# Performance work log

Hardware: AMD Instinct MI355X
Metric: run time of the kernel (lower is better)

## Reference

```python
import jax, jax.numpy as jnp
import numpy as np

EPS = 1e-5
MODES = 64
KERNEL = 25
PRED = 336
N_ENC = 2

def rmsnorm(x, w):
    return x * jax.lax.rsqrt(jnp.mean(jnp.square(x), axis=-1, keepdims=True) + EPS) * w

def ffn(x, w1, b1, w2, b2):
    return jax.nn.gelu(x @ w1 + b1, approximate=False) @ w2 + b2

def series_decomp(x):
    # moving average with zero padding (Conv1d, kernel=KERNEL, weight=1/KERNEL)
    pad = (KERNEL - 1) // 2
    xp = jnp.pad(x, ((0, 0), (pad, pad), (0, 0)))
    cs = jnp.cumsum(xp, axis=1)
    cs = jnp.concatenate([jnp.zeros_like(cs[:, :1]), cs], axis=1)
    t = (cs[:, KERNEL:, :] - cs[:, :-KERNEL, :]) / KERNEL  # [B,T,C]
    return x - t, t

def fourier_block(x, w, nw):
    # x: [B,T,C]; w: [MODES,C,2] learned complex weights; nw: [C] rms scale
    B, T, C = x.shape
    Xf = jnp.fft.rfft(x, axis=1)                      # [B,F,C] complex64
    mag = jnp.sum(Xf[:, 1:].real**2 + Xf[:, 1:].imag**2, axis=-1)  # [B,F-1]
    K = min(MODES, Xf.shape[1] - 1)
    _, idx = jax.lax.top_k(mag, K)
    idx = idx + 1                                      # skip DC, [B,K]
    Xsel = jnp.take_along_axis(Xf, idx[:, :, None], axis=1)  # [B,K,C]
    Wc = w[:K, :, 0] + 1j * w[:K, :, 1]               # [K,C]
    Ysel = Xsel * Wc[None]                             # [B,K,C]
    Yf = jnp.zeros_like(Xf).at[jnp.arange(B)[:, None], idx].set(Ysel)
    y = jnp.fft.irfft(Yf, n=T, axis=1)                 # [B,T,C]
    return rmsnorm(y, nw)

def setup_inputs() -> dict:
    key = jax.random.key(0)
    ks = iter(jax.random.split(key, 64))
    B, L, Cin, Cout, D, FF = 32, 1024, 8, 8, 512, 2048
    r = lambda *s: jax.random.normal(next(ks), s, dtype=jnp.float32) * 0.02
    z = lambda *s: jnp.zeros(s, dtype=jnp.float32)
    o = lambda *s: jnp.ones(s, dtype=jnp.float32)
    return {
        'x': jax.random.normal(next(ks), (B, L, Cin), dtype=jnp.float32),
        'enc_in_w': r(Cin, D), 'enc_in_b': z(D),
        'dec_in_w': r(Cin, D), 'dec_in_b': z(D),
        'enc_freq_w': r(N_ENC, MODES, D, 2), 'enc_freq_nw': o(N_ENC, D),
        'enc_n1': o(N_ENC, D), 'enc_n2': o(N_ENC, D),
        'enc_w1': r(N_ENC, D, FF), 'enc_b1': z(N_ENC, FF),
        'enc_w2': r(N_ENC, FF, D), 'enc_b2': z(N_ENC, D),
        'dec_freq_w': r(MODES, D, 2), 'dec_freq_nw': o(D),
        'dec_n1': o(D), 'dec_n2': o(D), 'dec_nx': o(D),
        'dec_cross_w': r(D, D), 'dec_cross_b': z(D),
        'dec_w1': r(D, FF), 'dec_b1': z(FF),
        'dec_w2': r(FF, D), 'dec_b2': z(D),
        'seas_w': r(D, Cout), 'seas_b': z(Cout),
        'tr_w1': r(D, FF), 'tr_b1': z(FF),
        'tr_w2': r(FF, Cout), 'tr_b2': z(Cout),
        'mix_w': r(Cout, Cout), 'mix_b': z(Cout),
        'qpos': jax.random.normal(next(ks), (1, PRED, D), dtype=jnp.float32) * 0.02,
    }

def reference(x, enc_in_w, enc_in_b, dec_in_w, dec_in_b,
              enc_freq_w, enc_freq_nw, enc_n1, enc_n2, enc_w1, enc_b1, enc_w2, enc_b2,
              dec_freq_w, dec_freq_nw, dec_n1, dec_n2, dec_nx, dec_cross_w, dec_cross_b,
              dec_w1, dec_b1, dec_w2, dec_b2, seas_w, seas_b,
              tr_w1, tr_b1, tr_w2, tr_b2, mix_w, mix_b, qpos):
    s, t = series_decomp(x)
    sez = s @ enc_in_w + enc_in_b                      # [B,L,D]
    for i in range(N_ENC):
        sez = sez + fourier_block(rmsnorm(sez, enc_n1[i]), enc_freq_w[i], enc_freq_nw[i])
        sez = sez + ffn(rmsnorm(sez, enc_n2[i]), enc_w1[i], enc_b1[i], enc_w2[i], enc_b2[i])
    memory = sez
    tgt = qpos + sez[:, -1:, :]                        # [B,PRED,D]
    # decoder layer
    m = jnp.mean(memory, axis=1, keepdims=True)        # [B,1,D]
    m = rmsnorm(m, dec_nx) @ dec_cross_w + dec_cross_b
    y = fourier_block(rmsnorm(tgt, dec_n1), dec_freq_w, dec_freq_nw)
    xd = tgt + y * jax.nn.sigmoid(m)
    xd = xd + ffn(rmsnorm(xd, dec_n2), dec_w1, dec_b1, dec_w2, dec_b2)
    sez_out = xd @ seas_w + seas_b                     # [B,PRED,Cout]
    tr = t @ dec_in_w + dec_in_b
    tr_out = ffn(tr[:, -1:, :], tr_w1, tr_b1, tr_w2, tr_b2)  # [B,1,Cout], broadcasts
    out = sez_out + tr_out
    return out @ mix_w + mix_b
```

## Files before the change

### kernel.cpp

```cpp
#include <hip/hip_runtime.h>
#include <hip/hip_fp16.h>
#include <math.h>

#define B_    32
#define L_    1024
#define D_    512
#define FF_   2048
#define PRED_ 336
#define ME_   (B_*L_)
#define MD_   (B_*PRED_)
#define EPS_  1e-5f

typedef _Float16 f16;
typedef _Float16 f16x8 __attribute__((ext_vector_type(8)));
typedef float    f32x4 __attribute__((ext_vector_type(4)));

__device__ __forceinline__ float wred64(float v) {
#pragma unroll
  for (int o = 32; o > 0; o >>= 1) v += __shfl_xor(v, o, 64);
  return v;
}
__device__ __forceinline__ double dwred64(double v) {
#pragma unroll
  for (int o = 32; o > 0; o >>= 1) v += __shfl_xor(v, o, 64);
  return v;
}
__device__ __forceinline__ float gelu_f(float x) {
  return 0.5f * x * (1.0f + erff(x * 0.7071067811865476f));
}
__device__ __forceinline__ void gl2lds16(const void* g, void* l) {
  __builtin_amdgcn_global_load_lds((const __attribute__((address_space(1))) void*)g,
                                   (__attribute__((address_space(3))) void*)l, 16, 0, 0);
}

__global__ void k_transpose_cast(const float* __restrict__ in, f16* __restrict__ out, int R, int C) {
  __shared__ float t[32][33];
  int c0 = blockIdx.x * 32, r0 = blockIdx.y * 32;
  int tx = threadIdx.x, ty = threadIdx.y;
#pragma unroll
  for (int j = ty; j < 32; j += 8) t[j][tx] = in[(size_t)(r0 + j) * C + c0 + tx];
  __syncthreads();
#pragma unroll
  for (int j = ty; j < 32; j += 8) out[(size_t)(c0 + j) * R + r0 + tx] = (f16)t[tx][j];
}

__global__ __launch_bounds__(256) void k_decomp_proj(const float* __restrict__ x,
    const float* __restrict__ w, const float* __restrict__ bias, float* __restrict__ sez) {
  int b = blockIdx.x, t0 = blockIdx.y * 128, tid = threadIdx.x;
  __shared__ float xs[152][8];
  __shared__ float st[128][8];
  __shared__ float wsm[8 * 512];
  __shared__ float bs[512];
  for (int i = tid; i < 152 * 8; i += 256) {
    int tt = i >> 3, c = i & 7; int tg = t0 - 12 + tt;
    xs[tt][c] = (tg >= 0 && tg < 1024) ? x[((size_t)b * 1024 + tg) * 8 + c] : 0.0f;
  }
  for (int i = tid; i < 4096; i += 256) wsm[i] = w[i];
  for (int i = tid; i < 512; i += 256) bs[i] = bias[i];
  __syncthreads();
  for (int i = tid; i < 1024; i += 256) {
    int t = i >> 3, c = i & 7;
    float s = 0.f;
#pragma unroll
    for (int j = 0; j < 25; ++j) s += xs[t + j][c];
    st[t][c] = xs[t + 12][c] - s / 25.0f;
  }
  __syncthreads();
#pragma unroll
  for (int g = 0; g < 2; ++g) {
    int d = tid + g * 256;
    float wb[8];
#pragma unroll
    for (int c = 0; c < 8; ++c) wb[c] = wsm[c * 512 + d];
    float bb = bs[d];
    for (int t = 0; t < 128; ++t) {
      float o = bb;
#pragma unroll
      for (int c = 0; c < 8; ++c) o += st[t][c] * wb[c];
      sez[((size_t)b * 1024 + t0 + t) * 512 + d] = o;
    }
  }
}

__global__ __launch_bounds__(512) void k_trend_trin(const float* __restrict__ x, const float* __restrict__ w,
    const float* __restrict__ bias, float* __restrict__ trin) {
  int b = blockIdx.x, tid = threadIdx.x;
  __shared__ float tl[8];
  if (tid < 8) {
    float s = 0.f;
    for (int j = 1011; j <= 1023; ++j) s += x[((size_t)b * 1024 + j) * 8 + tid];
    tl[tid] = s / 25.0f;
  }
  __syncthreads();
  float acc = bias[tid];
#pragma unroll
  for (int c = 0; c < 8; ++c) acc += tl[c] * w[c * 512 + tid];
  trin[b * 512 + tid] = acc;
}

__global__ __launch_bounds__(256) void k_rinv(const float* __restrict__ xin, float* __restrict__ rinv) {
  int row = blockIdx.x * 4 + (threadIdx.x >> 6), lane = threadIdx.x & 63;
  const float4* p = (const float4*)(xin + (size_t)row * 512);
  float4 a = p[lane * 2], b = p[lane * 2 + 1];
  float ss = a.x*a.x + a.y*a.y + a.z*a.z + a.w*a.w + b.x*b.x + b.y*b.y + b.z*b.z + b.w*b.w;
  ss = wred64(ss);
  if (lane == 0) rinv[row] = rsqrtf(ss * (1.0f / 512.0f) + EPS_);
}

__global__ __launch_bounds__(256) void k_rms_f16(const float* __restrict__ xin, const float* __restrict__ w,
    f16* __restrict__ out) {
  int row = blockIdx.x * 4 + (threadIdx.x >> 6), lane = threadIdx.x & 63;
  const float4* p = (const float4*)(xin + (size_t)row * 512);
  float4 a = p[lane * 2], b = p[lane * 2 + 1];
  float ss = a.x*a.x + a.y*a.y + a.z*a.z + a.w*a.w + b.x*b.x + b.y*b.y + b.z*b.z + b.w*b.w;
  ss = wred64(ss);
  float ri = rsqrtf(ss * (1.0f / 512.0f) + EPS_);
  const float4* wp = (const float4*)w;
  float4 wa = wp[lane * 2], wb = wp[lane * 2 + 1];
  float va[8] = {a.x, a.y, a.z, a.w, b.x, b.y, b.z, b.w};
  float wv[8] = {wa.x, wa.y, wa.z, wa.w, wb.x, wb.y, wb.z, wb.w};
  f16x8 o;
#pragma unroll
  for (int j = 0; j < 8; ++j) o[j] = (f16)((va[j] * ri) * wv[j]);
  *(f16x8*)(out + (size_t)row * 512 + lane * 8) = o;
}

#define IDX_(i) ((i) + ((i) >> 4))
__global__ __launch_bounds__(256) void k_fft_enc(const float* __restrict__ sez, const float* __restrict__ rinv,
    const float* __restrict__ n1, float* __restrict__ Xf) {
  int b = blockIdx.x, c0 = blockIdx.y * 4, tid = threadIdx.x;
  __shared__ double Zr[2][1088], Zi[2][1088];
  __shared__ double TWr[256], TWi[256];
  if (tid < 256) {
    double a = -6.283185307179586232 * (double)tid / 1024.0;
    TWr[tid] = cos(a); TWi[tid] = sin(a);
  }
  for (int i = tid; i < 4096; i += 256) {
    int t = i >> 2, cl = i & 3;
    float xv = (sez[((size_t)b * 1024 + t) * 512 + c0 + cl] * rinv[b * 1024 + t]) * n1[c0 + cl];
    int u = t, rt = 0;
#pragma unroll
    for (int d = 0; d < 5; ++d) { rt = (rt << 2) | (u & 3); u >>= 2; }
    if (cl & 1) Zi[cl >> 1][IDX_(rt)] = (double)xv; else Zr[cl >> 1][IDX_(rt)] = (double)xv;
  }
  __syncthreads();
#pragma unroll
  for (int s = 0; s < 5; ++s) {
    const int lh = 2 * s, h = 1 << lh;
#pragma unroll
    for (int qi = 0; qi < 2; ++qi) {
      int q = tid + qi * 256;
      int p = q >> 8, qq = q & 255;
      int j = qq & (h - 1), g = qq >> lh;
      int p0 = (g << (lh + 2)) + j;
      int i0 = IDX_(p0), i1 = IDX_(p0 + h), i2 = IDX_(p0 + 2 * h), i3 = IDX_(p0 + 3 * h);
      int tw = j << (8 - lh);
      double w1r = TWr[tw], w1i = TWi[tw];
      double w2r = w1r * w1r - w1i * w1i, w2i = 2.0 * w1r * w1i;
      double w3r = w2r * w1r - w2i * w1i, w3i = w2r * w1i + w2i * w1r;
      double Ar = Zr[p][i0], Ai = Zi[p][i0];
      double br = Zr[p][i1], bi = Zi[p][i1];
      double cr = Zr[p][i2], ci = Zi[p][i2];
      double dr = Zr[p][i3], di = Zi[p][i3];
      double Br = br * w1r - bi * w1i, Bi = br * w1i + bi * w1r;
      double Cr = cr * w2r - ci * w2i, Ci = cr * w2i + ci * w2r;
      double Dr = dr * w3r - di * w3i, Di = dr * w3i + di * w3r;
      double T0r = Ar + Cr, T0i = Ai + Ci;
      double T1r = Ar - Cr, T1i = Ai - Ci;
      double T2r = Br + Dr, T2i = Bi + Di;
      double T3r = Bi - Di, T3i = Dr - Br;
      Zr[p][i0] = T0r + T2r; Zi[p][i0] = T0i + T2i;
      Zr[p][i1] = T1r + T3r; Zi[p][i1] = T1i + T3i;
      Zr[p][i2] = T0r - T2r; Zi[p][i2] = T0i - T2i;
      Zr[p][i3] = T1r - T3r; Zi[p][i3] = T1i - T3i;
    }
    __syncthreads();
  }
  for (int i = tid; i < 513 * 2; i += 256) {
    int f = i >> 1, p = i & 1;
    int mf = (1024 - f) & 1023;
    double Ar = Zr[p][IDX_(f)], Ai = Zi[p][IDX_(f)], Br = Zr[p][IDX_(mf)], Bi = Zi[p][IDX_(mf)];
    float4 o;
    o.x = (float)(0.5 * (Ar + Br)); o.y = (float)(0.5 * (Ai - Bi));
    o.z = (float)(0.5 * (Ai + Bi)); o.w = (float)(0.5 * (Br - Ar));
    *(float4*)&Xf[(((size_t)b * 513 + f) * 512 + c0 + 2 * p) * 2] = o;
  }
}

__global__ __launch_bounds__(256) void k_mag(const float* __restrict__ Xf, double* __restrict__ mag, int F) {
  int b = blockIdx.x, f = blockIdx.y + 1, tid = threadIdx.x;
  const float2* row = (const float2*)(Xf + ((size_t)b * F + f) * 512 * 2);
  double s = 0;
  for (int c = tid; c < 512; c += 256) { float2 v = row[c]; s += (double)v.x * v.x + (double)v.y * v.y; }
  s = dwred64(s);
  __shared__ double ps[4];
  if ((tid & 63) == 0) ps[tid >> 6] = s;
  __syncthreads();
  if (tid == 0) mag[b * 513 + f] = ps[0] + ps[1] + ps[2] + ps[3];
}

__global__ __launch_bounds__(64) void k_topk(const double* __restrict__ mag, int* __restrict__ idx, int F) {
  int b = blockIdx.x, lane = threadIdx.x;
  double v[9];
#pragma unroll
  for (int j = 0; j < 9; ++j) {
    int s = j * 64 + lane;
    v[j] = (s >= 1 && s < F) ? mag[b * 513 + s] : -1e300;
  }
  for (int r = 0; r < 64; ++r) {
    double bv = -1e300; int bi = 0;
#pragma unroll
    for (int j = 0; j < 9; ++j)
      if (v[j] > bv) { bv = v[j]; bi = j * 64 + lane; }
#pragma unroll
    for (int o = 32; o > 0; o >>= 1) {
      double ov = __shfl_xor(bv, o, 64);
      int oi = __shfl_xor(bi, o, 64);
      if (ov > bv || (ov == bv && oi < bi)) { bv = ov; bi = oi; }
    }
    if (lane == 0) idx[b * 64 + r] = bi;
#pragma unroll
    for (int j = 0; j < 9; ++j)
      if (bi == j * 64 + lane) v[j] = -1e300;
  }
}

__global__ __launch_bounds__(512) void k_gather(const float* __restrict__ Xf, const int* __restrict__ idx,
    const float* __restrict__ fw, float* __restrict__ Ysel, int F, int T) {
  int b = blockIdx.x, k = blockIdx.y, c = threadIdx.x;
  int f = idx[b * 64 + k];
  float sc = (2 * f == T) ? (1.0f / (float)T) : (2.0f / (float)T);
  float2 xv = *(const float2*)&Xf[(((size_t)b * F + f) * 512 + c) * 2];
  float wr = fw[(k * 512 + c) * 2], wi = fw[(k * 512 + c) * 2 + 1];
  float yr = (xv.x * wr - xv.y * wi) * sc;
  float yi = (xv.x * wi + xv.y * wr) * sc;
  *(float2*)&Ysel[((size_t)(b * 64 + k) * 512 + c) * 2] = make_float2(yr, yi);
}

template <int T>
__global__ __launch_bounds__(256) void k_irfft(const float* __restrict__ Ysel, const int* __restrict__ idx,
    const float* __restrict__ nw, const float* __restrict__ sig,
    float* __restrict__ dst, int mode) {
  int b = blockIdx.x, t0 = blockIdx.y * 16, tid = threadIdx.x;
  int cq = tid & 127;
  int tg = tid >> 7;
  __shared__ float tcT[16][68], tsT[16][68];
  __shared__ int sidx[64];
  __shared__ float red[4][8];
  __shared__ float rfac[16];
  if (tid < 64) sidx[tid] = idx[b * 64 + tid];
  __syncthreads();
  for (int i = tid; i < 1024; i += 256) {
    int k = i >> 4, tt = i & 15;
    int m = (sidx[k] * (t0 + tt)) % T;
    float ang = (float)m * (float)(6.283185307179586232 / (double)T);
    tcT[tt][k] = cosf(ang);
    tsT[tt][k] = sinf(ang);
  }
  __syncthreads();
  float acc[8][4];
#pragma unroll
  for (int q = 0; q < 8; ++q)
#pragma unroll
    for (int j = 0; j < 4; ++j) acc[q][j] = 0.f;
  const float4* ys = (const float4*)Ysel + (size_t)b * 64 * 256 + 2 * cq;
  for (int k4 = 0; k4 < 64; k4 += 4) {
    float4 ya[4], yb[4];
#pragma unroll
    for (int kk = 0; kk < 4; ++kk) {
      ya[kk] = ys[(size_t)(k4 + kk) * 256];
      yb[kk] = ys[(size_t)(k4 + kk) * 256 + 1];
    }
#pragma unroll
    for (int q = 0; q < 8; ++q) {
      int tt = tg * 8 + q;
      float4 c4 = *(const float4*)&tcT[tt][k4];
      float4 s4 = *(const float4*)&tsT[tt][k4];
      acc[q][0] += ya[0].x * c4.x - ya[0].y * s4.x;
      acc[q][1] += ya[0].z * c4.x - ya[0].w * s4.x;
      acc[q][2] += yb[0].x * c4.x - yb[0].y * s4.x;
      acc[q][3] += yb[0].z * c4.x - yb[0].w * s4.x;
      acc[q][0] += ya[1].x * c4.y - ya[1].y * s4.y;
      acc[q][1] += ya[1].z * c4.y - ya[1].w * s4.y;
      acc[q][2] += yb[1].x * c4.y - yb[1].y * s4.y;
      acc[q][3] += yb[1].z * c4.y - yb[1].w * s4.y;
      acc[q][0] += ya[2].x * c4.z - ya[2].y * s4.z;
      acc[q][1] += ya[2].z * c4.z - ya[2].w * s4.z;
      acc[q][2] += yb[2].x * c4.z - yb[2].y * s4.z;
      acc[q][3] += yb[2].z * c4.z - yb[2].w * s4.z;
      acc[q][0] += ya[3].x * c4.w - ya[3].y * s4.w;
      acc[q][1] += ya[3].z * c4.w - ya[3].w * s4.w;
      acc[q][2] += yb[3].x * c4.w - yb[3].y * s4.w;
      acc[q][3] += yb[3].z * c4.w - yb[3].w * s4.w;
    }
  }
  int lane = tid & 63, wv = tid >> 6;
#pragma unroll
  for (int q = 0; q < 8; ++q) {
    float v = wred64(acc[q][0] * acc[q][0] + acc[q][1] * acc[q][1]
                   + acc[q][2] * acc[q][2] + acc[q][3] * acc[q][3]);
    if (lane == 0) red[wv][q] = v;
  }
  __syncthreads();
  if (tid < 16) {
    int tg2 = tid >> 3, q = tid & 7;
    float s = red[tg2 * 2][q] + red[tg2 * 2 + 1][q];
    rfac[tid] = rsqrtf(s * (1.0f / 512.0f) + EPS_);
  }
  __syncthreads();
  int c = 4 * cq;
  float4 wc = *(const float4*)&nw[c];
  float4 sg = (mode == 1) ? *(const float4*)&sig[b * 512 + c] : make_float4(1.f, 1.f, 1.f, 1.f);
  float* drow = dst + ((size_t)b * T + t0) * 512 + c;
#pragma unroll
  for (int q = 0; q < 8; ++q) {
    int tt = tg * 8 + q;
    float rf = rfac[tt];
    float4 cur = *(float4*)&drow[(size_t)tt * 512];
    float y0 = (acc[q][0] * rf) * wc.x;
    float y1 = (acc[q][1] * rf) * wc.y;
    float y2 = (acc[q][2] * rf) * wc.z;
    float y3 = (acc[q][3] * rf) * wc.w;
    cur.x += (mode == 1) ? y0 * sg.x : y0;
    cur.y += (mode == 1) ? y1 * sg.y : y1;
    cur.z += (mode == 1) ? y2 * sg.z : y2;
    cur.w += (mode == 1) ? y3 * sg.w : y3;
    *(float4*)&drow[(size_t)tt * 512] = cur;
  }
}

template <int MODE>
__global__ __launch_bounds__(256) void k_gemm(const f16* __restrict__ A, const f16* __restrict__ Bt,
    const float* __restrict__ bias, float* __restrict__ Cf, f16* __restrict__ Ch,
    int M, int N, int K) {
  __shared__ f16 lA[2][128][64];
  __shared__ f16 lB[2][128][64];
  int bm = blockIdx.x, bn = blockIdx.y;
  int tid = threadIdx.x, lane = tid & 63, w = tid >> 6;
  int wr = w >> 1, wcq = w & 1;
  f32x4 acc[4][4];
#pragma unroll
  for (int i = 0; i < 4; ++i)
#pragma unroll
    for (int j = 0; j < 4; ++j) acc[i][j] = (f32x4){0.f, 0.f, 0.f, 0.f};
  int lr = lane >> 3;
  int kk = (lane & 7) * 8;
  int nk = K >> 6;
  auto STAGE = [&](int buf, int kt) {
#pragma unroll
    for (int i = 0; i < 4; ++i) {
      int rt = (w * 4 + i) * 8;
      int rr = rt + lr;
      gl2lds16(A + (size_t)(bm * 128 + rr) * K + kt * 64 + kk, &lA[buf][rt][0]);
      gl2lds16(Bt + (size_t)(bn * 128 + rr) * K + kt * 64 + kk, &lB[buf][rt][0]);
    }
  };
  STAGE(0, 0);
  int cur = 0;
  for (int kt = 0; kt < nk; ++kt) {
    if (kt + 1 < nk) {
      STAGE(cur ^ 1, kt + 1);
      asm volatile("s_waitcnt vmcnt(8)\n\ts_barrier" ::: "memory");
    } else {
      asm volatile("s_waitcnt vmcnt(0)\n\ts_barrier" ::: "memory");
    }
#pragma unroll
    for (int ki = 0; ki < 2; ++ki) {
      f16x8 af[4], bf[4];
#pragma unroll
      for (int mi = 0; mi < 4; ++mi)
        af[mi] = *(const f16x8*)&lA[cur][wr * 64 + mi * 16 + (lane & 15)][ki * 32 + (lane >> 4) * 8];
#pragma unroll
      for (int ni = 0; ni < 4; ++ni)
        bf[ni] = *(const f16x8*)&lB[cur][wcq * 64 + ni * 16 + (lane & 15)][ki * 32 + (lane >> 4) * 8];
#pragma unroll
      for (int mi = 0; mi < 4; ++mi)
#pragma unroll
        for (int ni = 0; ni < 4; ++ni)
          acc[mi][ni] = __builtin_amdgcn_mfma_f32_16x16x32_f16(af[mi], bf[ni], acc[mi][ni], 0, 0, 0);
    }
    asm volatile("s_barrier" ::: "memory");
    cur ^= 1;
  }
  int cbase = bn * 128 + wcq * 64;
  int rbase = bm * 128 + wr * 64;
#pragma unroll
  for (int mi = 0; mi < 4; ++mi)
#pragma unroll
    for (int ni = 0; ni < 4; ++ni) {
      int cg = cbase + ni * 16 + (lane & 15);
      float bv = bias[cg];
#pragma unroll
      for (int q = 0; q < 4; ++q) {
        int rg = rbase + mi * 16 + (lane >> 4) * 4 + q;
        float val = acc[mi][ni][q] + bv;
        if (MODE == 0) Ch[(size_t)rg * N + cg] = (f16)gelu_f(val);
        else           Cf[(size_t)rg * N + cg] += val;
      }
    }
}

__global__ __launch_bounds__(256) void k_mc_part(const float* __restrict__ sez, float* __restrict__ mcp) {
  int b = blockIdx.x, ch = blockIdx.y, tid = threadIdx.x;
  for (int d = tid; d < 512; d += 256) {
    float s = 0.f;
    for (int t = 0; t < 128; ++t) s += sez[((size_t)b * 1024 + ch * 128 + t) * 512 + d];
    mcp[((size_t)b * 8 + ch) * 512 + d] = s;
  }
}
__global__ __launch_bounds__(512) void k_mc_fin(const float* __restrict__ mcp, const float* __restrict__ nx,
    const float* __restrict__ Wc, const float* __restrict__ cb, float* __restrict__ sig) {
  int b = blockIdx.x, d = threadIdx.x;
  float m = 0.f;
#pragma unroll
  for (int ch = 0; ch < 8; ++ch) m += mcp[((size_t)b * 8 + ch) * 512 + d];
  m *= (1.0f / 1024.0f);
  float ss = wred64(m * m);
  __shared__ float ps[8];
  __shared__ float mn[512];
  int lane = d & 63, wv = d >> 6;
  if (lane == 0) ps[wv] = ss;
  __syncthreads();
  float tot = 0.f;
#pragma unroll
  for (int i = 0; i < 8; ++i) tot += ps[i];
  float ri = rsqrtf(tot * (1.0f / 512.0f) + EPS_);
  mn[d] = (m * ri) * nx[d];
  __syncthreads();
  float accv = cb[d];
  for (int e = 0; e < 512; ++e) accv += mn[e] * Wc[(size_t)e * 512 + d];
  sig[b * 512 + d] = 1.0f / (1.0f + expf(-accv));
}

__global__ __launch_bounds__(512) void k_make_tgt(const float* __restrict__ sez, const float* __restrict__ qpos,
    const float* __restrict__ n1, float* __restrict__ tgt, float* __restrict__ tgt_n,
    float* __restrict__ rinvd) {
  int row = blockIdx.x, d = threadIdx.x;
  int b = row / 336, p = row % 336;
  float v = qpos[(size_t)p * 512 + d] + sez[((size_t)b * 1024 + 1023) * 512 + d];
  tgt[(size_t)row * 512 + d] = v;
  float ss = wred64(v * v);
  __shared__ float ps[8];
  if ((d & 63) == 0) ps[d >> 6] = ss;
  __syncthreads();
  float t = 0.f;
#pragma unroll
  for (int i = 0; i < 8; ++i) t += ps[i];
  float ri = rsqrtf(t * (1.0f / 512.0f) + EPS_);
  tgt_n[(size_t)row * 512 + d] = (v * ri) * n1[d];
  if (d == 0) rinvd[row] = ri;
}

__global__ void k_dtab(float* __restrict__ dtt) {
  int f = blockIdx.x;
  for (int t = threadIdx.x; t < 336; t += 256) {
    float cv = 0.f, sv = 0.f;
    if (f < 169) {
      int m = (f * t) % 336;
      double a = 6.283185307179586232 * (double)m / 336.0;
      cv = (float)cos(a); sv = (float)sin(a);
    }
    dtt[((size_t)t * 176 + f) * 2]     = cv;
    dtt[((size_t)t * 176 + f) * 2 + 1] = sv;
  }
}
__global__ __launch_bounds__(512) void k_dft_dec(const float* __restrict__ tgt_n,
    const float* __restrict__ dtt, float* __restrict__ Xf) {
  int b = blockIdx.x, f0 = blockIdx.y * 4, c = threadIdx.x;
  float ar[4], ai[4];
#pragma unroll
  for (int i = 0; i < 4; ++i) { ar[i] = 0.f; ai[i] = 0.f; }
  const float* trow = tgt_n + (size_t)b * 336 * 512 + c;
  for (int t = 0; t < 336; ++t) {
    float xv = trow[(size_t)t * 512];
    const float* tab = dtt + ((size_t)t * 176 + f0) * 2;
#pragma unroll
    for (int ff = 0; ff < 4; ++ff) {
      ar[ff] += xv * tab[ff * 2];
      ai[ff] -= xv * tab[ff * 2 + 1];
    }
  }
#pragma unroll
  for (int ff = 0; ff < 4; ++ff) {
    int f = f0 + ff;
    if (f < 169)
      *(float2*)&Xf[(((size_t)b * 169 + f) * 512 + c) * 2] = make_float2(ar[ff], ai[ff]);
  }
}

__global__ __launch_bounds__(256) void k_tr_h(const float* __restrict__ trin, const float* __restrict__ w1,
    const float* __restrict__ b1, float* __restrict__ H) {
  int b = blockIdx.x, j0 = blockIdx.y * 512, tid = threadIdx.x;
  __shared__ float xs[512];
  for (int i = tid; i < 512; i += 256) xs[i] = trin[b * 512 + i];
  __syncthreads();
  int j = j0 + tid;
  float h0 = b1[j], h1 = b1[j + 256];
  const float* wp = w1 + j;
#pragma unroll 4
  for (int e = 0; e < 512; ++e) {
    float xe = xs[e];
    h0 += xe * wp[(size_t)e * 2048];
    h1 += xe * wp[(size_t)e * 2048 + 256];
  }
  H[b * 2048 + j] = gelu_f(h0);
  H[b * 2048 + j + 256] = gelu_f(h1);
}

__global__ __launch_bounds__(256) void k_tr_red(const float* __restrict__ H, const float* __restrict__ w2,
    const float* __restrict__ b2, float* __restrict__ trout) {
  int b = blockIdx.x, tid = threadIdx.x;
  __shared__ float red[4][8];
  float part[8];
#pragma unroll
  for (int co = 0; co < 8; ++co) part[co] = 0.f;
#pragma unroll
  for (int jj = 0; jj < 8; ++jj) {
    int j = tid + jj * 256;
    float g = H[b * 2048 + j];
    float4 wa = *(const float4*)&w2[(size_t)j * 8];
    float4 wb = *(const float4*)&w2[(size_t)j * 8 + 4];
    part[0] += g * wa.x; part[1] += g * wa.y; part[2] += g * wa.z; part[3] += g * wa.w;
    part[4] += g * wb.x; part[5] += g * wb.y; part[6] += g * wb.z; part[7] += g * wb.w;
  }
  int lane = tid & 63, wv = tid >> 6;
#pragma unroll
  for (int co = 0; co < 8; ++co) {
    float v = wred64(part[co]);
    if (lane == 0) red[wv][co] = v;
  }
  __syncthreads();
  if (tid < 8) trout[b * 8 + tid] = red[0][tid] + red[1][tid] + red[2][tid] + red[3][tid] + b2[tid];
}

__global__ __launch_bounds__(256) void k_head(const float* __restrict__ xd, const float* __restrict__ sw,
    const float* __restrict__ sb, const float* __restrict__ trout, const float* __restrict__ mw,
    const float* __restrict__ mb, float* __restrict__ outp) {
  int row = blockIdx.x, tid = threadIdx.x;
  int b = row / 336;
  __shared__ float wsm[512 * 8];
  __shared__ float red[4][8];
  __shared__ float srow[8];
  for (int i = tid; i < 4096; i += 256) wsm[i] = sw[i];
  __syncthreads();
  float part[8];
#pragma unroll
  for (int co = 0; co < 8; ++co) part[co] = 0.f;
#pragma unroll
  for (int g = 0; g < 2; ++g) {
    int d = tid + g * 256;
    float xv = xd[(size_t)row * 512 + d];
#pragma unroll
    for (int co = 0; co < 8; ++co) part[co] += xv * wsm[d * 8 + co];
  }
  int lane = tid & 63, wv = tid >> 6;
#pragma unroll
  for (int co = 0; co < 8; ++co) {
    float v = wred64(part[co]);
    if (lane == 0) red[wv][co] = v;
  }
  __syncthreads();
  if (tid == 0) {
#pragma unroll
    for (int co = 0; co < 8; ++co)
      srow[co] = red[0][co] + red[1][co] + red[2][co] + red[3][co] + sb[co] + trout[b * 8 + co];
  }
  __syncthreads();
  if (tid < 8) {
    float o = mb[tid];
#pragma unroll
    for (int co = 0; co < 8; ++co) o += srow[co] * mw[co * 8 + tid];
    outp[(size_t)row * 8 + tid] = o;
  }
}

extern "C" void kernel_launch(void* const* d_in, const int* in_sizes, int n_in,
                              void* d_out, int out_size, void* d_ws, size_t ws_size,
                              hipStream_t stream) {
  const float* x        = (const float*)d_in[0];
  const float* enc_in_w = (const float*)d_in[1];
  const float* enc_in_b = (const float*)d_in[2];
  const float* dec_in_w = (const float*)d_in[3];
  const float* dec_in_b = (const float*)d_in[4];
  const float* enc_fw   = (const float*)d_in[5];
  const float* enc_fnw  = (const float*)d_in[6];
  const float* enc_n1   = (const float*)d_in[7];
  const float* enc_n2   = (const float*)d_in[8];
  const float* enc_w1   = (const float*)d_in[9];
  const float* enc_b1   = (const float*)d_in[10];
  const float* enc_w2   = (const float*)d_in[11];
  const float* enc_b2   = (const float*)d_in[12];
  const float* dec_fw   = (const float*)d_in[13];
  const float* dec_fnw  = (const float*)d_in[14];
  const float* dec_n1   = (const float*)d_in[15];
  const float* dec_n2   = (const float*)d_in[16];
  const float* dec_nx   = (const float*)d_in[17];
  const float* dec_cw   = (const float*)d_in[18];
  const float* dec_cb   = (const float*)d_in[19];
  const float* dec_w1   = (const float*)d_in[20];
  const float* dec_b1   = (const float*)d_in[21];
  const float* dec_w2   = (const float*)d_in[22];
  const float* dec_b2   = (const float*)d_in[23];
  const float* seas_w   = (const float*)d_in[24];
  const float* seas_b   = (const float*)d_in[25];
  const float* tr_w1    = (const float*)d_in[26];
  const float* tr_b1    = (const float*)d_in[27];
  const float* tr_w2    = (const float*)d_in[28];
  const float* tr_b2    = (const float*)d_in[29];
  const float* mix_w    = (const float*)d_in[30];
  const float* mix_b    = (const float*)d_in[31];
  const float* qpos     = (const float*)d_in[32];
  float* outp = (float*)d_out;
  (void)in_sizes; (void)n_in; (void)out_size; (void)ws_size;

  char* wsb = (char*)d_ws;
  size_t off = 0;
  auto take = [&](size_t n) -> char* {
    char* p = wsb + off;
    off = (off + n + 255) & ~(size_t)255;
    return p;
  };
  float*  sez   = (float*)take((size_t)ME_ * 512 * 4);
  f16*    xn    = (f16*)take((size_t)ME_ * 512 * 2);
  const size_t XF_BYTES = (size_t)32 * 513 * 512 * 2 * 4;
  char*   arena = take(XF_BYTES + (size_t)32 * 64 * 512 * 2 * 4);
  float*  Xf    = (float*)arena;
  f16*    hbuf  = (f16*)arena;
  float*  Ysel  = (float*)(arena + XF_BYTES);
  float*  tgt   = (float*)take((size_t)MD_ * 512 * 4);
  float*  tgt_n = (float*)take((size_t)MD_ * 512 * 4);
  double* mag   = (double*)take((size_t)32 * 513 * 8);
  int*    idx   = (int*)take((size_t)32 * 64 * 4);
  float*  rinvp = (float*)take((size_t)ME_ * 4);
  float*  rinvd = (float*)take((size_t)MD_ * 4);
  float*  mcp   = (float*)take((size_t)32 * 8 * 512 * 4);
  float*  sig   = (float*)take((size_t)32 * 512 * 4);
  float*  trin  = (float*)take((size_t)32 * 512 * 4);
  float*  trout = (float*)take((size_t)32 * 8 * 4);
  float*  trH   = (float*)take((size_t)32 * 2048 * 4);
  float*  dtt   = (float*)take((size_t)336 * 176 * 2 * 4);
  f16*    w1t   = (f16*)take((size_t)2 * 2048 * 512 * 2);
  f16*    w2t   = (f16*)take((size_t)2 * 512 * 2048 * 2);
  f16*    dw1t  = (f16*)take((size_t)2048 * 512 * 2);
  f16*    dw2t  = (f16*)take((size_t)512 * 2048 * 2);

  k_transpose_cast<<<dim3(64, 16), dim3(32, 8), 0, stream>>>(enc_w1, w1t, 512, 2048);
  k_transpose_cast<<<dim3(64, 16), dim3(32, 8), 0, stream>>>(enc_w1 + 512 * 2048, w1t + 2048 * 512, 512, 2048);
  k_transpose_cast<<<dim3(16, 64), dim3(32, 8), 0, stream>>>(enc_w2, w2t, 2048, 512);
  k_transpose_cast<<<dim3(16, 64), dim3(32, 8), 0, stream>>>(enc_w2 + 2048 * 512, w2t + 512 * 2048, 2048, 512);
  k_transpose_cast<<<dim3(64, 16), dim3(32, 8), 0, stream>>>(dec_w1, dw1t, 512, 2048);
  k_transpose_cast<<<dim3(16, 64), dim3(32, 8), 0, stream>>>(dec_w2, dw2t, 2048, 512);

  k_decomp_proj<<<dim3(32, 8), 256, 0, stream>>>(x, enc_in_w, enc_in_b, sez);
  k_trend_trin<<<32, 512, 0, stream>>>(x, dec_in_w, dec_in_b, trin);

  k_tr_h<<<dim3(32, 4), 256, 0, stream>>>(trin, tr_w1, tr_b1, trH);
  k_tr_red<<<32, 256, 0, stream>>>(trH, tr_w2, tr_b2, trout);

  for (int i = 0; i < 2; ++i) {
    k_rinv<<<ME_ / 4, 256, 0, stream>>>(sez, rinvp);
    k_fft_enc<<<dim3(32, 128), 256, 0, stream>>>(sez, rinvp, enc_n1 + i * 512, Xf);
    k_mag<<<dim3(32, 512), 256, 0, stream>>>(Xf, mag, 513);
    k_topk<<<32, 64, 0, stream>>>(mag, idx, 513);
    k_gather<<<dim3(32, 64), 512, 0, stream>>>(Xf, idx, enc_fw + (size_t)i * 64 * 512 * 2, Ysel, 513, 1024);
    k_irfft<1024><<<dim3(32, 64), 256, 0, stream>>>(Ysel, idx, enc_fnw + i * 512, nullptr, sez, 0);
    k_rms_f16<<<ME_ / 4, 256, 0, stream>>>(sez, enc_n2 + i * 512, xn);
    for (int ck = 0; ck < 2; ++ck) {
      const f16* Ax = xn + (size_t)ck * 16384 * 512;
      float* Cx = sez + (size_t)ck * 16384 * 512;
      k_gemm<0><<<dim3(128, 16), 256, 0, stream>>>(Ax, w1t + (size_t)i * 2048 * 512, enc_b1 + i * 2048,
                                                   nullptr, hbuf, 16384, 2048, 512);
      k_gemm<1><<<dim3(128, 4), 256, 0, stream>>>(hbuf, w2t + (size_t)i * 512 * 2048, enc_b2 + i * 512,
                                                  Cx, nullptr, 16384, 512, 2048);
    }
  }

  k_mc_part<<<dim3(32, 8), 256, 0, stream>>>(sez, mcp);
  k_mc_fin<<<32, 512, 0, stream>>>(mcp, dec_nx, dec_cw, dec_cb, sig);
  k_make_tgt<<<MD_, 512, 0, stream>>>(sez, qpos, dec_n1, tgt, tgt_n, rinvd);
  k_dtab<<<176, 256, 0, stream>>>(dtt);
  k_dft_dec<<<dim3(32, 43), 512, 0, stream>>>(tgt_n, dtt, Xf);
  k_mag<<<dim3(32, 168), 256, 0, stream>>>(Xf, mag, 169);
  k_topk<<<32, 64, 0, stream>>>(mag, idx, 169);
  k_gather<<<dim3(32, 64), 512, 0, stream>>>(Xf, idx, dec_fw, Ysel, 169, 336);
  k_irfft<336><<<dim3(32, 21), 256, 0, stream>>>(Ysel, idx, dec_fnw, sig, tgt, 1);
  k_rms_f16<<<MD_ / 4, 256, 0, stream>>>(tgt, dec_n2, xn);
  k_gemm<0><<<dim3(84, 16), 256, 0, stream>>>(xn, dw1t, dec_b1, nullptr, hbuf, MD_, 2048, 512);
  k_gemm<1><<<dim3(84, 4), 256, 0, stream>>>(hbuf, dw2t, dec_b2, tgt, nullptr, MD_, 512, 2048);

  k_head<<<MD_, 256, 0, stream>>>(tgt, seas_w, seas_b, trout, mix_w, mix_b, outp);
}
```

Baseline: 1.524 ms.

## Swizzle GEMM LDS layout and compute decoder DFT in double precision

The GEMM's LDS staging and fragment reads now XOR-swizzle the 16-byte column chunk with the row index. The goal is to remove bank conflicts in the MFMA operand reads. Separately, the decoder DFT table and accumulators move from float to double, which raises precision (likely for top-k mode-selection stability) at the cost of slower FP64 arithmetic and twice the table bandwidth. The two changes are unrelated.

```diff
diff --git a/kernel.cpp b/kernel.cpp
--- a/kernel.cpp
+++ b/kernel.cpp
@@ -344,15 +344,15 @@
 #pragma unroll
     for (int j = 0; j < 4; ++j) acc[i][j] = (f32x4){0.f, 0.f, 0.f, 0.f};
   int lr = lane >> 3;
-  int kk = (lane & 7) * 8;
+  int kswz = ((lane & 7) ^ lr) * 8;
   int nk = K >> 6;
   auto STAGE = [&](int buf, int kt) {
 #pragma unroll
     for (int i = 0; i < 4; ++i) {
       int rt = (w * 4 + i) * 8;
       int rr = rt + lr;
-      gl2lds16(A + (size_t)(bm * 128 + rr) * K + kt * 64 + kk, &lA[buf][rt][0]);
-      gl2lds16(Bt + (size_t)(bn * 128 + rr) * K + kt * 64 + kk, &lB[buf][rt][0]);
+      gl2lds16(A + (size_t)(bm * 128 + rr) * K + kt * 64 + kswz, &lA[buf][rt][0]);
+      gl2lds16(Bt + (size_t)(bn * 128 + rr) * K + kt * 64 + kswz, &lB[buf][rt][0]);
     }
   };
   STAGE(0, 0);
@@ -367,12 +367,14 @@
 #pragma unroll
     for (int ki = 0; ki < 2; ++ki) {
       f16x8 af[4], bf[4];
+      int clog = ki * 4 + (lane >> 4);
+      int cphys = (clog ^ (lane & 7)) * 8;
 #pragma unroll
       for (int mi = 0; mi < 4; ++mi)
-        af[mi] = *(const f16x8*)&lA[cur][wr * 64 + mi * 16 + (lane & 15)][ki * 32 + (lane >> 4) * 8];
+        af[mi] = *(const f16x8*)&lA[cur][wr * 64 + mi * 16 + (lane & 15)][cphys];
 #pragma unroll
       for (int ni = 0; ni < 4; ++ni)
-        bf[ni] = *(const f16x8*)&lB[cur][wcq * 64 + ni * 16 + (lane & 15)][ki * 32 + (lane >> 4) * 8];
+        bf[ni] = *(const f16x8*)&lB[cur][wcq * 64 + ni * 16 + (lane & 15)][cphys];
 #pragma unroll
       for (int mi = 0; mi < 4; ++mi)
 #pragma unroll
@@ -451,40 +453,40 @@
   if (d == 0) rinvd[row] = ri;
 }
 
-__global__ void k_dtab(float* __restrict__ dtt) {
+__global__ void k_dtab(double* __restrict__ dtt) {
   int f = blockIdx.x;
   for (int t = threadIdx.x; t < 336; t += 256) {
-    float cv = 0.f, sv = 0.f;
+    double cv = 0.0, sv = 0.0;
     if (f < 169) {
       int m = (f * t) % 336;
       double a = 6.283185307179586232 * (double)m / 336.0;
-      cv = (float)cos(a); sv = (float)sin(a);
+      cv = cos(a); sv = sin(a);
     }
     dtt[((size_t)t * 176 + f) * 2]     = cv;
     dtt[((size_t)t * 176 + f) * 2 + 1] = sv;
   }
 }
 __global__ __launch_bounds__(512) void k_dft_dec(const float* __restrict__ tgt_n,
-    const float* __restrict__ dtt, float* __restrict__ Xf) {
+    const double* __restrict__ dtt, float* __restrict__ Xf) {
   int b = blockIdx.x, f0 = blockIdx.y * 4, c = threadIdx.x;
-  float ar[4], ai[4];
-#pragma unroll
-  for (int i = 0; i < 4; ++i) { ar[i] = 0.f; ai[i] = 0.f; }
+  double ar[4], ai[4];
+#pragma unroll
+  for (int i = 0; i < 4; ++i) { ar[i] = 0.0; ai[i] = 0.0; }
   const float* trow = tgt_n + (size_t)b * 336 * 512 + c;
   for (int t = 0; t < 336; ++t) {
-    float xv = trow[(size_t)t * 512];
-    const float* tab = dtt + ((size_t)t * 176 + f0) * 2;
+    double xd = (double)trow[(size_t)t * 512];
+    const double* tab = dtt + ((size_t)t * 176 + f0) * 2;
 #pragma unroll
     for (int ff = 0; ff < 4; ++ff) {
-      ar[ff] += xv * tab[ff * 2];
-      ai[ff] -= xv * tab[ff * 2 + 1];
+      ar[ff] += xd * tab[ff * 2];
+      ai[ff] -= xd * tab[ff * 2 + 1];
     }
   }
 #pragma unroll
   for (int ff = 0; ff < 4; ++ff) {
     int f = f0 + ff;
     if (f < 169)
-      *(float2*)&Xf[(((size_t)b * 169 + f) * 512 + c) * 2] = make_float2(ar[ff], ai[ff]);
+      *(float2*)&Xf[(((size_t)b * 169 + f) * 512 + c) * 2] = make_float2((float)ar[ff], (float)ai[ff]);
   }
 }
 
@@ -638,7 +640,7 @@
   float*  trin  = (float*)take((size_t)32 * 512 * 4);
   float*  trout = (float*)take((size_t)32 * 8 * 4);
   float*  trH   = (float*)take((size_t)32 * 2048 * 4);
-  float*  dtt   = (float*)take((size_t)336 * 176 * 2 * 4);
+  double* dtt   = (double*)take((size_t)336 * 176 * 2 * 8);
   f16*    w1t   = (f16*)take((size_t)2 * 2048 * 512 * 2);
   f16*    w2t   = (f16*)take((size_t)2 * 512 * 2048 * 2);
   f16*    dw1t  = (f16*)take((size_t)2048 * 512 * 2);
```

Result: faster. 1.424 ms (-6.6%).
